# Performance work log

Measured on AMD Instinct MI355X. Metric: run time of the kernel, lower is better.

## Reference

```python
import jax, jax.numpy as jnp
import numpy as np

B, C, H, W = 1, 192, 96, 96


def setup_inputs() -> dict:
    key = jax.random.key(0)
    k1, k2 = jax.random.split(key, 2)
    latent_feats = jax.random.normal(k1, (B, C, H, W), dtype=jnp.float32)
    refined_feats = jax.random.normal(k2, (B, C, H, W), dtype=jnp.float32)
    w_4 = jnp.ones((1, C, H, W), dtype=jnp.float32)
    w_5 = jnp.ones((1, C, H, W), dtype=jnp.float32)
    return {"latent_feats": latent_feats, "refined_feats": refined_feats, "w_4": w_4, "w_5": w_5}


def reference(latent_feats, refined_feats, w_4, w_5):
    # b == 1 (torch.mm requires 2D operands, so the original only works for batch 1)
    hw = H * W
    lat = (latent_feats * w_4)[0].reshape(C, hw)          # [c, hw]
    ref = refined_feats[0].reshape(C, hw)                 # [c, hw]
    scores = jnp.einsum('cn,cm->nm', ref, lat)            # [(hw)_ref, (hw)_lat]
    attn = jax.nn.softmax(scores, axis=-2)                # softmax over rows (dim -2)
    ctx = jnp.einsum('cn,nm->cm', lat, attn)              # [c, hw]
    return refined_feats * w_5 + ctx.reshape(1, C, H, W)
```

## Files before the change

### kernel.cpp

```cpp
#include <hip/hip_runtime.h>
#include <stdint.h>


#define NQ 9216
#define NC 192
#define FR 1769472
#define M0 25.0f

typedef short    bfrag  __attribute__((ext_vector_type(8)));
typedef _Float16 hfrag  __attribute__((ext_vector_type(8)));
typedef short    sfrag4 __attribute__((ext_vector_type(4)));
typedef float    facc16 __attribute__((ext_vector_type(16)));

__device__ __forceinline__ short f2bf(float x) {
    uint32_t u = __builtin_bit_cast(uint32_t, x);
    u = (u + 0x7fffu + ((u >> 16) & 1u)) >> 16;
    return (short)u;
}
__device__ __forceinline__ float bf2f(short s) {
    uint32_t u = ((uint32_t)(uint16_t)s) << 16;
    return __builtin_bit_cast(float, u);
}
__device__ __forceinline__ int cvtpk_bf16(float lo, float hi) {
    int r;
    asm("v_cvt_pk_bf16_f32 %0, %1, %2" : "=v"(r) : "v"(lo), "v"(hi));
    return r;
}
__device__ __forceinline__ bfrag words_to_frag(int w0, int w1, int w2, int w3) {
    union { int i[4]; bfrag f; } u;
    u.i[0] = w0; u.i[1] = w1; u.i[2] = w2; u.i[3] = w3;
    return u.f;
}
__device__ __forceinline__ void gload_lds16(const void* g, void* l) {
    __builtin_amdgcn_global_load_lds(
        (__attribute__((address_space(1))) const void*)(uintptr_t)g,
        (__attribute__((address_space(3))) void*)(uint32_t)(uintptr_t)l,
        16, 0, 0);
}

__global__ __launch_bounds__(256) void InterGate_prep(
    const float* __restrict__ latent, const float* __restrict__ refined,
    const float* __restrict__ w4,
    short* __restrict__ Qf, short* __restrict__ KV)
{
    const int wid  = blockIdx.x * 4 + (threadIdx.x >> 6);
    const int lane = threadIdx.x & 63;
    const int l32  = lane & 31, h = lane >> 5;

    if (wid < 3456) {
        const int qw = wid / 12, t = wid % 12;
        const int q  = qw * 32 + l32;
        const int c0 = t * 16 + h * 8;
        hfrag hv;
        #pragma unroll
        for (int i = 0; i < 8; i++) {
            size_t idx = (size_t)(c0 + i) * NQ + q;
            hv[i] = (_Float16)(latent[idx] * w4[idx]);
        }
        *(hfrag*)(void*)(Qf + ((size_t)wid * 64 + lane) * 8) = hv;
    } else if (wid < 6912) {
        const int u  = wid - 3456;
        const int kg = u / 24, r = u % 24;
        const int n2 = r / 12, t = r % 12;
        const int key = kg * 64 + n2 * 32 + l32;
        const int c0  = t * 16 + h * 8;
        hfrag hv;
        #pragma unroll
        for (int i = 0; i < 8; i++) {
            size_t idx = (size_t)(c0 + i) * NQ + key;
            hv[i] = (_Float16)refined[idx];
        }
        *(hfrag*)(void*)(KV + (size_t)kg * 24576 + ((n2 * 12 + t) * 64 + lane) * 8) = hv;
    } else {
        const int u  = wid - 6912;
        const int kg = u / 24, r = u % 24;
        const int t  = r / 6, cb = r % 6;
        const int c  = cb * 32 + l32;
        const int k0 = kg * 64 + t * 16 + h * 8;
        bfrag bv;
        #pragma unroll
        for (int i = 0; i < 8; i++) {
            size_t idx = (size_t)c * NQ + k0 + i;
            bv[i] = f2bf(latent[idx] * w4[idx]);
        }
        *(bfrag*)(void*)(KV + (size_t)kg * 24576 + 12288 + ((t * 6 + cb) * 64 + lane) * 8) = bv;
    }
}

__global__ __launch_bounds__(512, 2) void InterGate_flash(
    const short* __restrict__ Qf, const short* __restrict__ KV,
    short* __restrict__ Opart, float* __restrict__ l_ws, int KS)
{
    __shared__ __align__(16) short kv[2][24576];

    const int tid  = threadIdx.x;
    const int lane = tid & 63, w = tid >> 6;
    const int l32  = lane & 31, h = lane >> 5;
    const int qt   = blockIdx.x, ks = blockIdx.y;

    const int base = 144 / KS, rem = 144 % KS;
    const int start = ks * base + (ks < rem ? ks : rem);
    const int cnt   = base + (ks < rem ? 1 : 0);

    const int qw = qt * 8 + w;
    hfrag qf[12];
    #pragma unroll
    for (int t = 0; t < 12; t++)
        qf[t] = *(const hfrag*)(const void*)(Qf + (((size_t)qw * 12 + t) * 64 + lane) * 8);

    facc16 O[6];
    #pragma unroll
    for (int cb = 0; cb < 6; cb++)
        #pragma unroll
        for (int j = 0; j < 16; j++) O[cb][j] = 0.f;
    float lsum = 0.f;

    {
        const char* src = (const char*)(KV + (size_t)start * 24576) + lane * 16;
        char* dst = (char*)&kv[0][0];
        #pragma unroll
        for (int j = 0; j < 6; j++) {
            const int u = w * 6 + j;
            gload_lds16(src + u * 1024, dst + u * 1024);
        }
    }

    for (int kt = 0; kt < cnt; kt++) {
        __syncthreads();
        const int cur = kt & 1;
        if (kt + 1 < cnt) {
            const char* src = (const char*)(KV + (size_t)(start + kt + 1) * 24576) + lane * 16;
            char* dst = (char*)&kv[cur ^ 1][0];
            #pragma unroll
            for (int j = 0; j < 6; j++) {
                const int u = w * 6 + j;
                gload_lds16(src + u * 1024, dst + u * 1024);
            }
        }
        const short* kb = &kv[cur][0];

        #pragma unroll
        for (int n2 = 0; n2 < 2; n2++) {
            facc16 S;
            #pragma unroll
            for (int j = 0; j < 16; j++) S[j] = 0.f;
            #pragma unroll
            for (int t = 0; t < 12; t++) {
                hfrag kf = *(const hfrag*)(const void*)(kb + (n2 * 12 + t) * 512 + lane * 8);
                S = __builtin_amdgcn_mfma_f32_32x32x16_f16(kf, qf[t], S, 0, 0, 0);
            }

            float p[16];
            #pragma unroll
            for (int j = 0; j < 16; j++) {
                p[j] = __expf(S[j] - M0);
                lsum += p[j];
            }
            int cp[8], sw[8];
            #pragma unroll
            for (int a = 0; a < 8; a++) cp[a] = cvtpk_bf16(p[2 * a], p[2 * a + 1]);
            #pragma unroll
            for (int a = 0; a < 8; a++) sw[a] = __shfl_xor(cp[a], 32);
            const bool lo = (h == 0);

            #pragma unroll
            for (int T = 0; T < 2; T++) {
                const int b0 = T * 4;
                bfrag pf = words_to_frag(
                    lo ? cp[b0 + 0] : sw[b0 + 2],
                    lo ? cp[b0 + 1] : sw[b0 + 3],
                    lo ? sw[b0 + 0] : cp[b0 + 2],
                    lo ? sw[b0 + 1] : cp[b0 + 3]);
                const int ksp = 2 * n2 + T;
                #pragma unroll
                for (int cb = 0; cb < 6; cb++) {
                    bfrag vf = *(const bfrag*)(const void*)(kb + 12288 + (ksp * 6 + cb) * 512 + lane * 8);
                    O[cb] = __builtin_amdgcn_mfma_f32_32x32x16_bf16(vf, pf, O[cb], 0, 0, 0);
                }
            }
        }
    }

    const int q = qt * 256 + w * 32 + l32;
    short* orow = Opart + ((size_t)ks * NQ + q) * NC;
    #pragma unroll
    for (int cb = 0; cb < 6; cb++) {
        #pragma unroll
        for (int g = 0; g < 4; g++) {
            const int c0 = cb * 32 + 8 * g + 4 * h;
            sfrag4 s4;
            #pragma unroll
            for (int r = 0; r < 4; r++) s4[r] = f2bf(O[cb][4 * g + r]);
            *(sfrag4*)(void*)(orow + c0) = s4;
        }
    }
    float ltot = lsum + __shfl_xor(lsum, 32);
    if (h == 0) l_ws[(size_t)ks * NQ + q] = ltot;
}

__global__ __launch_bounds__(256) void InterGate_combine(
    const short* __restrict__ Opart, const float* __restrict__ l_ws,
    const float* __restrict__ refined, const float* __restrict__ w5,
    float* __restrict__ out, int KS)
{
    __shared__ float ctx[32][193];
    __shared__ float sInv[32];
    const int qt = blockIdx.x, tid = threadIdx.x;

    if (tid < 32) {
        const int q = qt * 32 + tid;
        float L = 0.f;
        for (int ks = 0; ks < KS; ks++) L += l_ws[(size_t)ks * NQ + q];
        sInv[tid] = 1.f / L;
    }
    __syncthreads();

    for (int u = tid; u < 768; u += 256) {
        const int ql = u / 24, c0 = (u % 24) * 8;
        float acc[8] = {0.f, 0.f, 0.f, 0.f, 0.f, 0.f, 0.f, 0.f};
        for (int ks = 0; ks < KS; ks++) {
            bfrag pk = *(const bfrag*)(const void*)&Opart[((size_t)ks * NQ + qt * 32 + ql) * NC + c0];
            #pragma unroll
            for (int j = 0; j < 8; j++) acc[j] += bf2f(pk[j]);
        }
        const float inv = sInv[ql];
        #pragma unroll
        for (int j = 0; j < 8; j++) ctx[ql][c0 + j] = acc[j] * inv;
    }
    __syncthreads();

    for (int u = tid; u < 6144; u += 256) {
        const int c = u / 32, qx = u % 32;
        size_t o = (size_t)c * NQ + qt * 32 + qx;
        out[o] = refined[o] * w5[o] + ctx[qx][c];
    }
}

extern "C" void kernel_launch(void* const* d_in, const int* in_sizes, int n_in,
                              void* d_out, int out_size, void* d_ws, size_t ws_size,
                              hipStream_t stream)
{
    (void)in_sizes; (void)n_in; (void)out_size;
    const float* latent  = (const float*)d_in[0];
    const float* refined = (const float*)d_in[1];
    const float* w4      = (const float*)d_in[2];
    const float* w5      = (const float*)d_in[3];
    float* out = (float*)d_out;

    short* Qf = (short*)d_ws;
    short* KV = Qf + FR;
    const size_t basebytes = (size_t)3 * FR * 2;

    const int opts[4] = {7, 4, 2, 1};
    int KS = 0;
    for (int i = 0; i < 4; i++) {
        size_t need = basebytes + (size_t)opts[i] * ((size_t)NQ * NC * 2 + (size_t)NQ * 4);
        if (need <= ws_size) { KS = opts[i]; break; }
    }
    if (KS == 0) return;

    short* Opart = (short*)((char*)d_ws + basebytes);
    float* l_ws  = (float*)((char*)d_ws + basebytes + (size_t)KS * NQ * NC * 2);

    InterGate_prep<<<2592, 256, 0, stream>>>(latent, refined, w4, Qf, KV);
    dim3 fg(36, KS);
    InterGate_flash<<<fg, 512, 0, stream>>>(Qf, KV, Opart, l_ws, KS);
    InterGate_combine<<<288, 256, 0, stream>>>(Opart, l_ws, refined, w5, out, KS);
}
```

Measured before the change: 97.15 us.

## Process two query tiles per wave, fold log2e into Q, drop P shuffles

Each wave now computes two 32-query tiles, so every K/V fragment read from LDS feeds two MFMAs. The block shrinks to 256 threads with launch bounds (256,1) to free registers for the doubled accumulators. Q is pre-scaled by log2e so the softmax uses raw v_exp_f32. The V layout in prep is permuted so the packed P values feed the second MFMA directly, removing the cross-half shuffles. The cost is higher register pressure and lower occupancy: one 4-wave block per CU instead of two 8-wave blocks.

Result: slower. 99.65 us (+2.6%).

```diff
diff --git a/kernel.cpp b/kernel.cpp
--- a/kernel.cpp
+++ b/kernel.cpp
@@ -5,7 +5,8 @@
 #define NQ 9216
 #define NC 192
 #define FR 1769472
-#define M0 25.0f
+#define LOG2E 1.4426950408889634f
+#define M0L 36.06737602f
 
 typedef short    bfrag  __attribute__((ext_vector_type(8)));
 typedef _Float16 hfrag  __attribute__((ext_vector_type(8)));
@@ -24,6 +25,11 @@
 __device__ __forceinline__ int cvtpk_bf16(float lo, float hi) {
     int r;
     asm("v_cvt_pk_bf16_f32 %0, %1, %2" : "=v"(r) : "v"(lo), "v"(hi));
+    return r;
+}
+__device__ __forceinline__ float exp2_raw(float x) {
+    float r;
+    asm("v_exp_f32 %0, %1" : "=v"(r) : "v"(x));
     return r;
 }
 __device__ __forceinline__ bfrag words_to_frag(int w0, int w1, int w2, int w3) {
@@ -55,7 +61,7 @@
         #pragma unroll
         for (int i = 0; i < 8; i++) {
             size_t idx = (size_t)(c0 + i) * NQ + q;
-            hv[i] = (_Float16)(latent[idx] * w4[idx]);
+            hv[i] = (_Float16)(latent[idx] * w4[idx] * LOG2E);
         }
         *(hfrag*)(void*)(Qf + ((size_t)wid * 64 + lane) * 8) = hv;
     } else if (wid < 6912) {
@@ -76,18 +82,19 @@
         const int kg = u / 24, r = u % 24;
         const int t  = r / 6, cb = r % 6;
         const int c  = cb * 32 + l32;
-        const int k0 = kg * 64 + t * 16 + h * 8;
+        const int k0 = kg * 64 + t * 16 + 4 * h;
         bfrag bv;
         #pragma unroll
         for (int i = 0; i < 8; i++) {
-            size_t idx = (size_t)c * NQ + k0 + i;
+            const int row = k0 + (i & 3) + 8 * (i >> 2);
+            size_t idx = (size_t)c * NQ + row;
             bv[i] = f2bf(latent[idx] * w4[idx]);
         }
         *(bfrag*)(void*)(KV + (size_t)kg * 24576 + 12288 + ((t * 6 + cb) * 64 + lane) * 8) = bv;
     }
 }
 
-__global__ __launch_bounds__(512, 2) void InterGate_flash(
+__global__ __launch_bounds__(256, 1) void InterGate_flash(
     const short* __restrict__ Qf, const short* __restrict__ KV,
     short* __restrict__ Opart, float* __restrict__ l_ws, int KS)
 {
@@ -102,100 +109,107 @@
     const int start = ks * base + (ks < rem ? ks : rem);
     const int cnt   = base + (ks < rem ? 1 : 0);
 
-    const int qw = qt * 8 + w;
-    hfrag qf[12];
+    const int qw = qt * 8 + w * 2;
+    hfrag qa[12], qb[12];
     #pragma unroll
-    for (int t = 0; t < 12; t++)
-        qf[t] = *(const hfrag*)(const void*)(Qf + (((size_t)qw * 12 + t) * 64 + lane) * 8);
-
-    facc16 O[6];
+    for (int t = 0; t < 12; t++) {
+        qa[t] = *(const hfrag*)(const void*)(Qf + (((size_t)qw * 12 + t) * 64 + lane) * 8);
+        qb[t] = *(const hfrag*)(const void*)(Qf + (((size_t)(qw + 1) * 12 + t) * 64 + lane) * 8);
+    }
+
+    facc16 OA[6], OB[6];
     #pragma unroll
-    for (int cb = 0; cb < 6; cb++)
-        #pragma unroll
-        for (int j = 0; j < 16; j++) O[cb][j] = 0.f;
-    float lsum = 0.f;
+    for (int cb = 0; cb < 6; cb++) {
+        #pragma unroll
+        for (int j = 0; j < 16; j++) { OA[cb][j] = 0.f; OB[cb][j] = 0.f; }
+    }
+    float lsA = 0.f, lsB = 0.f;
 
     {
-        const char* src = (const char*)(KV + (size_t)start * 24576) + lane * 16;
-        char* dst = (char*)&kv[0][0];
-        #pragma unroll
-        for (int j = 0; j < 6; j++) {
-            const int u = w * 6 + j;
-            gload_lds16(src + u * 1024, dst + u * 1024);
-        }
+        const char* src = (const char*)(KV + (size_t)start * 24576) + w * 12288 + lane * 16;
+        char* dst = (char*)&kv[0][0] + w * 12288;
+        #pragma unroll
+        for (int j = 0; j < 12; j++)
+            gload_lds16(src + j * 1024, dst + j * 1024);
     }
 
     for (int kt = 0; kt < cnt; kt++) {
         __syncthreads();
         const int cur = kt & 1;
         if (kt + 1 < cnt) {
-            const char* src = (const char*)(KV + (size_t)(start + kt + 1) * 24576) + lane * 16;
-            char* dst = (char*)&kv[cur ^ 1][0];
-            #pragma unroll
-            for (int j = 0; j < 6; j++) {
-                const int u = w * 6 + j;
-                gload_lds16(src + u * 1024, dst + u * 1024);
-            }
+            const char* src = (const char*)(KV + (size_t)(start + kt + 1) * 24576) + w * 12288 + lane * 16;
+            char* dst = (char*)&kv[cur ^ 1][0] + w * 12288;
+            #pragma unroll
+            for (int j = 0; j < 12; j++)
+                gload_lds16(src + j * 1024, dst + j * 1024);
         }
         const short* kb = &kv[cur][0];
 
         #pragma unroll
         for (int n2 = 0; n2 < 2; n2++) {
-            facc16 S;
-            #pragma unroll
-            for (int j = 0; j < 16; j++) S[j] = 0.f;
+            facc16 S0, S1;
+            #pragma unroll
+            for (int j = 0; j < 16; j++) { S0[j] = 0.f; S1[j] = 0.f; }
             #pragma unroll
             for (int t = 0; t < 12; t++) {
                 hfrag kf = *(const hfrag*)(const void*)(kb + (n2 * 12 + t) * 512 + lane * 8);
-                S = __builtin_amdgcn_mfma_f32_32x32x16_f16(kf, qf[t], S, 0, 0, 0);
-            }
-
-            float p[16];
+                S0 = __builtin_amdgcn_mfma_f32_32x32x16_f16(kf, qa[t], S0, 0, 0, 0);
+                S1 = __builtin_amdgcn_mfma_f32_32x32x16_f16(kf, qb[t], S1, 0, 0, 0);
+            }
+
+            float pa[16], pb[16];
             #pragma unroll
             for (int j = 0; j < 16; j++) {
-                p[j] = __expf(S[j] - M0);
-                lsum += p[j];
-            }
-            int cp[8], sw[8];
-            #pragma unroll
-            for (int a = 0; a < 8; a++) cp[a] = cvtpk_bf16(p[2 * a], p[2 * a + 1]);
-            #pragma unroll
-            for (int a = 0; a < 8; a++) sw[a] = __shfl_xor(cp[a], 32);
-            const bool lo = (h == 0);
+                pa[j] = exp2_raw(S0[j] - M0L);
+                pb[j] = exp2_raw(S1[j] - M0L);
+            }
+            lsA += (((pa[0]+pa[1])+(pa[2]+pa[3]))+((pa[4]+pa[5])+(pa[6]+pa[7])))
+                 + (((pa[8]+pa[9])+(pa[10]+pa[11]))+((pa[12]+pa[13])+(pa[14]+pa[15])));
+            lsB += (((pb[0]+pb[1])+(pb[2]+pb[3]))+((pb[4]+pb[5])+(pb[6]+pb[7])))
+                 + (((pb[8]+pb[9])+(pb[10]+pb[11]))+((pb[12]+pb[13])+(pb[14]+pb[15])));
+            int cpA[8], cpB[8];
+            #pragma unroll
+            for (int a = 0; a < 8; a++) {
+                cpA[a] = cvtpk_bf16(pa[2 * a], pa[2 * a + 1]);
+                cpB[a] = cvtpk_bf16(pb[2 * a], pb[2 * a + 1]);
+            }
 
             #pragma unroll
             for (int T = 0; T < 2; T++) {
-                const int b0 = T * 4;
-                bfrag pf = words_to_frag(
-                    lo ? cp[b0 + 0] : sw[b0 + 2],
-                    lo ? cp[b0 + 1] : sw[b0 + 3],
-                    lo ? sw[b0 + 0] : cp[b0 + 2],
-                    lo ? sw[b0 + 1] : cp[b0 + 3]);
-                const int ksp = 2 * n2 + T;
+                bfrag pfA = words_to_frag(cpA[4*T], cpA[4*T+1], cpA[4*T+2], cpA[4*T+3]);
+                bfrag pfB = words_to_frag(cpB[4*T], cpB[4*T+1], cpB[4*T+2], cpB[4*T+3]);
+                const int ksp = n2 * 2 + T;
                 #pragma unroll
                 for (int cb = 0; cb < 6; cb++) {
                     bfrag vf = *(const bfrag*)(const void*)(kb + 12288 + (ksp * 6 + cb) * 512 + lane * 8);
-                    O[cb] = __builtin_amdgcn_mfma_f32_32x32x16_bf16(vf, pf, O[cb], 0, 0, 0);
+                    OA[cb] = __builtin_amdgcn_mfma_f32_32x32x16_bf16(vf, pfA, OA[cb], 0, 0, 0);
+                    OB[cb] = __builtin_amdgcn_mfma_f32_32x32x16_bf16(vf, pfB, OB[cb], 0, 0, 0);
                 }
             }
         }
     }
 
-    const int q = qt * 256 + w * 32 + l32;
-    short* orow = Opart + ((size_t)ks * NQ + q) * NC;
+    const int q0 = qt * 256 + w * 64 + l32;
+    short* rowA = Opart + ((size_t)ks * NQ + q0) * NC;
+    short* rowB = rowA + (size_t)32 * NC;
     #pragma unroll
     for (int cb = 0; cb < 6; cb++) {
         #pragma unroll
         for (int g = 0; g < 4; g++) {
             const int c0 = cb * 32 + 8 * g + 4 * h;
-            sfrag4 s4;
-            #pragma unroll
-            for (int r = 0; r < 4; r++) s4[r] = f2bf(O[cb][4 * g + r]);
-            *(sfrag4*)(void*)(orow + c0) = s4;
-        }
-    }
-    float ltot = lsum + __shfl_xor(lsum, 32);
-    if (h == 0) l_ws[(size_t)ks * NQ + q] = ltot;
+            sfrag4 sa, sb;
+            #pragma unroll
+            for (int r = 0; r < 4; r++) { sa[r] = f2bf(OA[cb][4*g+r]); sb[r] = f2bf(OB[cb][4*g+r]); }
+            *(sfrag4*)(void*)(rowA + c0) = sa;
+            *(sfrag4*)(void*)(rowB + c0) = sb;
+        }
+    }
+    float la = lsA + __shfl_xor(lsA, 32);
+    float lb = lsB + __shfl_xor(lsB, 32);
+    if (h == 0) {
+        l_ws[(size_t)ks * NQ + q0]      = la;
+        l_ws[(size_t)ks * NQ + q0 + 32] = lb;
+    }
 }
 
 __global__ __launch_bounds__(256) void InterGate_combine(
@@ -264,6 +278,6 @@
 
     InterGate_prep<<<2592, 256, 0, stream>>>(latent, refined, w4, Qf, KV);
     dim3 fg(36, KS);
-    InterGate_flash<<<fg, 512, 0, stream>>>(Qf, KV, Opart, l_ws, KS);
+    InterGate_flash<<<fg, 256, 0, stream>>>(Qf, KV, Opart, l_ws, KS);
     InterGate_combine<<<288, 256, 0, stream>>>(Opart, l_ws, refined, w5, out, KS);
 }
```

## Stream V fragments through registers, shrink key tile, use raw exp2 softmax

Applied to the files above, without the earlier changes.

Splits the packed K/V workspace into separate K and V arrays and reorders the V layout so the P fragment can be built from the MFMA output without cross-half lane shuffles. The flash kernel now stages only K in LDS with 32-key tiles, and prefetches V fragments directly from global memory into registers, overlapping those loads with the PV MFMAs. The log2e factor is folded into Q during prep, so the softmax can use the raw v_exp_f32 instruction, and the row sum becomes a tree reduction. Split-K options are doubled to match the smaller tiles. The trade-offs are more register pressure, more global traffic for V per block, and more partial outputs for the combine kernel to sum.

Result: slower. 121.6 us (+25.2%).

```diff
diff --git a/kernel.cpp b/kernel.cpp
--- a/kernel.cpp
+++ b/kernel.cpp
@@ -5,7 +5,8 @@
 #define NQ 9216
 #define NC 192
 #define FR 1769472
-#define M0 25.0f
+#define LOG2E 1.4426950408889634f
+#define M0L 36.06737602f
 
 typedef short    bfrag  __attribute__((ext_vector_type(8)));
 typedef _Float16 hfrag  __attribute__((ext_vector_type(8)));
@@ -24,6 +25,11 @@
 __device__ __forceinline__ int cvtpk_bf16(float lo, float hi) {
     int r;
     asm("v_cvt_pk_bf16_f32 %0, %1, %2" : "=v"(r) : "v"(lo), "v"(hi));
+    return r;
+}
+__device__ __forceinline__ float exp2_raw(float x) {
+    float r;
+    asm("v_exp_f32 %0, %1" : "=v"(r) : "v"(x));
     return r;
 }
 __device__ __forceinline__ bfrag words_to_frag(int w0, int w1, int w2, int w3) {
@@ -41,7 +47,7 @@
 __global__ __launch_bounds__(256) void InterGate_prep(
     const float* __restrict__ latent, const float* __restrict__ refined,
     const float* __restrict__ w4,
-    short* __restrict__ Qf, short* __restrict__ KV)
+    short* __restrict__ Qf, short* __restrict__ Karr, short* __restrict__ Varr)
 {
     const int wid  = blockIdx.x * 4 + (threadIdx.x >> 6);
     const int lane = threadIdx.x & 63;
@@ -55,14 +61,13 @@
         #pragma unroll
         for (int i = 0; i < 8; i++) {
             size_t idx = (size_t)(c0 + i) * NQ + q;
-            hv[i] = (_Float16)(latent[idx] * w4[idx]);
+            hv[i] = (_Float16)(latent[idx] * w4[idx] * LOG2E);
         }
         *(hfrag*)(void*)(Qf + ((size_t)wid * 64 + lane) * 8) = hv;
     } else if (wid < 6912) {
-        const int u  = wid - 3456;
-        const int kg = u / 24, r = u % 24;
-        const int n2 = r / 12, t = r % 12;
-        const int key = kg * 64 + n2 * 32 + l32;
+        const int u = wid - 3456;
+        const int g = u / 12, t = u % 12;
+        const int key = g * 32 + l32;
         const int c0  = t * 16 + h * 8;
         hfrag hv;
         #pragma unroll
@@ -70,35 +75,37 @@
             size_t idx = (size_t)(c0 + i) * NQ + key;
             hv[i] = (_Float16)refined[idx];
         }
-        *(hfrag*)(void*)(KV + (size_t)kg * 24576 + ((n2 * 12 + t) * 64 + lane) * 8) = hv;
+        *(hfrag*)(void*)(Karr + ((size_t)u * 64 + lane) * 8) = hv;
     } else {
-        const int u  = wid - 6912;
-        const int kg = u / 24, r = u % 24;
-        const int t  = r / 6, cb = r % 6;
+        const int u = wid - 6912;
+        const int g = u / 12, r = u % 12;
+        const int T = r / 6, cb = r % 6;
         const int c  = cb * 32 + l32;
-        const int k0 = kg * 64 + t * 16 + h * 8;
+        const int k0 = g * 32 + T * 16 + 4 * h;
         bfrag bv;
         #pragma unroll
         for (int i = 0; i < 8; i++) {
-            size_t idx = (size_t)c * NQ + k0 + i;
+            const int row = k0 + (i & 3) + 8 * (i >> 2);
+            size_t idx = (size_t)c * NQ + row;
             bv[i] = f2bf(latent[idx] * w4[idx]);
         }
-        *(bfrag*)(void*)(KV + (size_t)kg * 24576 + 12288 + ((t * 6 + cb) * 64 + lane) * 8) = bv;
+        *(bfrag*)(void*)(Varr + ((size_t)u * 64 + lane) * 8) = bv;
     }
 }
 
 __global__ __launch_bounds__(512, 2) void InterGate_flash(
-    const short* __restrict__ Qf, const short* __restrict__ KV,
+    const short* __restrict__ Qf, const short* __restrict__ Karr,
+    const short* __restrict__ Varr,
     short* __restrict__ Opart, float* __restrict__ l_ws, int KS)
 {
-    __shared__ __align__(16) short kv[2][24576];
+    __shared__ __align__(16) short kbuf[2][6144];
 
     const int tid  = threadIdx.x;
     const int lane = tid & 63, w = tid >> 6;
     const int l32  = lane & 31, h = lane >> 5;
     const int qt   = blockIdx.x, ks = blockIdx.y;
 
-    const int base = 144 / KS, rem = 144 % KS;
+    const int base = 288 / KS, rem = 288 % KS;
     const int start = ks * base + (ks < rem ? ks : rem);
     const int cnt   = base + (ks < rem ? 1 : 0);
 
@@ -116,12 +123,17 @@
     float lsum = 0.f;
 
     {
-        const char* src = (const char*)(KV + (size_t)start * 24576) + lane * 16;
-        char* dst = (char*)&kv[0][0];
-        #pragma unroll
-        for (int j = 0; j < 6; j++) {
-            const int u = w * 6 + j;
-            gload_lds16(src + u * 1024, dst + u * 1024);
+        const char* src = (const char*)(Karr + (size_t)start * 6144) + lane * 16;
+        char* dst = (char*)&kbuf[0][0];
+        for (int u = w; u < 12; u += 8) gload_lds16(src + u * 1024, dst + u * 1024);
+    }
+    bfrag vg0[6], vg1[6];
+    {
+        const short* vb = Varr + (size_t)start * 6144;
+        #pragma unroll
+        for (int cb = 0; cb < 6; cb++) {
+            vg0[cb] = *(const bfrag*)(const void*)(vb + cb * 512 + lane * 8);
+            vg1[cb] = *(const bfrag*)(const void*)(vb + 3072 + cb * 512 + lane * 8);
         }
     }
 
@@ -129,60 +141,53 @@
         __syncthreads();
         const int cur = kt & 1;
         if (kt + 1 < cnt) {
-            const char* src = (const char*)(KV + (size_t)(start + kt + 1) * 24576) + lane * 16;
-            char* dst = (char*)&kv[cur ^ 1][0];
-            #pragma unroll
-            for (int j = 0; j < 6; j++) {
-                const int u = w * 6 + j;
-                gload_lds16(src + u * 1024, dst + u * 1024);
-            }
-        }
-        const short* kb = &kv[cur][0];
-
-        #pragma unroll
-        for (int n2 = 0; n2 < 2; n2++) {
-            facc16 S;
-            #pragma unroll
-            for (int j = 0; j < 16; j++) S[j] = 0.f;
-            #pragma unroll
-            for (int t = 0; t < 12; t++) {
-                hfrag kf = *(const hfrag*)(const void*)(kb + (n2 * 12 + t) * 512 + lane * 8);
-                S = __builtin_amdgcn_mfma_f32_32x32x16_f16(kf, qf[t], S, 0, 0, 0);
-            }
-
-            float p[16];
-            #pragma unroll
-            for (int j = 0; j < 16; j++) {
-                p[j] = __expf(S[j] - M0);
-                lsum += p[j];
-            }
-            int cp[8], sw[8];
-            #pragma unroll
-            for (int a = 0; a < 8; a++) cp[a] = cvtpk_bf16(p[2 * a], p[2 * a + 1]);
-            #pragma unroll
-            for (int a = 0; a < 8; a++) sw[a] = __shfl_xor(cp[a], 32);
-            const bool lo = (h == 0);
-
-            #pragma unroll
-            for (int T = 0; T < 2; T++) {
-                const int b0 = T * 4;
-                bfrag pf = words_to_frag(
-                    lo ? cp[b0 + 0] : sw[b0 + 2],
-                    lo ? cp[b0 + 1] : sw[b0 + 3],
-                    lo ? sw[b0 + 0] : cp[b0 + 2],
-                    lo ? sw[b0 + 1] : cp[b0 + 3]);
-                const int ksp = 2 * n2 + T;
-                #pragma unroll
-                for (int cb = 0; cb < 6; cb++) {
-                    bfrag vf = *(const bfrag*)(const void*)(kb + 12288 + (ksp * 6 + cb) * 512 + lane * 8);
-                    O[cb] = __builtin_amdgcn_mfma_f32_32x32x16_bf16(vf, pf, O[cb], 0, 0, 0);
-                }
-            }
-        }
-    }
-
-    const int q = qt * 256 + w * 32 + l32;
-    short* orow = Opart + ((size_t)ks * NQ + q) * NC;
+            const char* src = (const char*)(Karr + (size_t)(start + kt + 1) * 6144) + lane * 16;
+            char* dst = (char*)&kbuf[cur ^ 1][0];
+            for (int u = w; u < 12; u += 8) gload_lds16(src + u * 1024, dst + u * 1024);
+        }
+        const short* kb = &kbuf[cur][0];
+
+        facc16 S;
+        #pragma unroll
+        for (int j = 0; j < 16; j++) S[j] = 0.f;
+        #pragma unroll
+        for (int t = 0; t < 12; t++) {
+            hfrag kf = *(const hfrag*)(const void*)(kb + t * 512 + lane * 8);
+            S = __builtin_amdgcn_mfma_f32_32x32x16_f16(kf, qf[t], S, 0, 0, 0);
+        }
+
+        float p[16];
+        #pragma unroll
+        for (int j = 0; j < 16; j++) p[j] = exp2_raw(S[j] - M0L);
+        lsum += (((p[0]+p[1])+(p[2]+p[3]))+((p[4]+p[5])+(p[6]+p[7])))
+              + (((p[8]+p[9])+(p[10]+p[11]))+((p[12]+p[13])+(p[14]+p[15])));
+        int cp[8];
+        #pragma unroll
+        for (int a = 0; a < 8; a++) cp[a] = cvtpk_bf16(p[2 * a], p[2 * a + 1]);
+
+        const short* vnext = Varr + (size_t)(start + kt + 1) * 6144;
+        bfrag pf0 = words_to_frag(cp[0], cp[1], cp[2], cp[3]);
+        #pragma unroll
+        for (int cb = 0; cb < 6; cb++)
+            O[cb] = __builtin_amdgcn_mfma_f32_32x32x16_bf16(vg0[cb], pf0, O[cb], 0, 0, 0);
+        if (kt + 1 < cnt) {
+            #pragma unroll
+            for (int cb = 0; cb < 6; cb++)
+                vg0[cb] = *(const bfrag*)(const void*)(vnext + cb * 512 + lane * 8);
+        }
+        bfrag pf1 = words_to_frag(cp[4], cp[5], cp[6], cp[7]);
+        #pragma unroll
+        for (int cb = 0; cb < 6; cb++)
+            O[cb] = __builtin_amdgcn_mfma_f32_32x32x16_bf16(vg1[cb], pf1, O[cb], 0, 0, 0);
+        if (kt + 1 < cnt) {
+            #pragma unroll
+            for (int cb = 0; cb < 6; cb++)
+                vg1[cb] = *(const bfrag*)(const void*)(vnext + 3072 + cb * 512 + lane * 8);
+        }
+    }
+
+    const int q0 = qt * 256 + w * 32 + l32;
+    short* row = Opart + ((size_t)ks * NQ + q0) * NC;
     #pragma unroll
     for (int cb = 0; cb < 6; cb++) {
         #pragma unroll
@@ -191,11 +196,11 @@
             sfrag4 s4;
             #pragma unroll
             for (int r = 0; r < 4; r++) s4[r] = f2bf(O[cb][4 * g + r]);
-            *(sfrag4*)(void*)(orow + c0) = s4;
-        }
-    }
-    float ltot = lsum + __shfl_xor(lsum, 32);
-    if (h == 0) l_ws[(size_t)ks * NQ + q] = ltot;
+            *(sfrag4*)(void*)(row + c0) = s4;
+        }
+    }
+    float lt = lsum + __shfl_xor(lsum, 32);
+    if (h == 0) l_ws[(size_t)ks * NQ + q0] = lt;
 }
 
 __global__ __launch_bounds__(256) void InterGate_combine(
@@ -247,13 +252,14 @@
     const float* w5      = (const float*)d_in[3];
     float* out = (float*)d_out;
 
-    short* Qf = (short*)d_ws;
-    short* KV = Qf + FR;
+    short* Qf   = (short*)d_ws;
+    short* Karr = Qf + FR;
+    short* Varr = Karr + FR;
     const size_t basebytes = (size_t)3 * FR * 2;
 
-    const int opts[4] = {7, 4, 2, 1};
+    const int opts[5] = {14, 8, 4, 2, 1};
     int KS = 0;
-    for (int i = 0; i < 4; i++) {
+    for (int i = 0; i < 5; i++) {
         size_t need = basebytes + (size_t)opts[i] * ((size_t)NQ * NC * 2 + (size_t)NQ * 4);
         if (need <= ws_size) { KS = opts[i]; break; }
     }
@@ -262,8 +268,8 @@
     short* Opart = (short*)((char*)d_ws + basebytes);
     float* l_ws  = (float*)((char*)d_ws + basebytes + (size_t)KS * NQ * NC * 2);
 
-    InterGate_prep<<<2592, 256, 0, stream>>>(latent, refined, w4, Qf, KV);
+    InterGate_prep<<<2592, 256, 0, stream>>>(latent, refined, w4, Qf, Karr, Varr);
     dim3 fg(36, KS);
-    InterGate_flash<<<fg, 512, 0, stream>>>(Qf, KV, Opart, l_ws, KS);
+    InterGate_flash<<<fg, 512, 0, stream>>>(Qf, Karr, Varr, Opart, l_ws, KS);
     InterGate_combine<<<288, 256, 0, stream>>>(Opart, l_ws, refined, w5, out, KS);
 }
```
